# Kernel optimization log

Hardware: AMD Instinct MI355X
Metric: run time of the kernel (lower is better)

## Reference

```python
import jax, jax.numpy as jnp
import numpy as np
from jax import lax

TEMP = 0.1  # softmax_temp default in forward


def _conv(x, w, b):
    y = lax.conv_general_dilated(x, w, (1, 1), 'VALID',
                                 dimension_numbers=('NCHW', 'OIHW', 'NCHW'))
    return y + b[None, :, None, None]


def _avg_pool2(x):
    # AvgPool2d(2,2), floor mode (VALID window)
    s = lax.reduce_window(x, 0.0, lax.add, (1, 1, 2, 2), (1, 1, 2, 2), 'VALID')
    return s / 4.0


def _cnn(x, c1w, c1b, c2w, c2b, c3w, c3b, dw, db):
    x = _avg_pool2(jax.nn.relu(_conv(x, c1w, c1b)))   # (N,8,13,13)
    x = _avg_pool2(jax.nn.relu(_conv(x, c2w, c2b)))   # (N,16,5,5)
    x = _avg_pool2(jax.nn.relu(_conv(x, c3w, c3b)))   # (N,32,1,1)
    x = x.reshape(x.shape[0], -1)                      # (N,32)
    logits = x @ dw.T + db                             # (N,10)
    return jax.nn.softmax(logits, axis=1)


def _digit_to_rule(p):
    # p: (N,10) -> (N,6)
    return jnp.stack([p[:, 8], p[:, 4] + p[:, 6], p[:, 0] + p[:, 2],
                      p[:, 7] + p[:, 9], p[:, 5], p[:, 1] + p[:, 3]], axis=1)


def setup_inputs() -> dict:
    key = jax.random.key(0)
    ks = jax.random.split(key, 10)
    B, T, D, C, H, W = 256, 8, 4, 1, 28, 28
    sc = 0.1
    return {
        'sequences': jax.random.normal(ks[0], (B, T, D, C, H, W), jnp.float32),
        'conv1_w': jax.random.normal(ks[1], (8, 1, 3, 3), jnp.float32) * sc,
        'conv1_b': jax.random.normal(ks[2], (8,), jnp.float32) * sc,
        'conv2_w': jax.random.normal(ks[3], (16, 8, 3, 3), jnp.float32) * sc,
        'conv2_b': jax.random.normal(ks[4], (16,), jnp.float32) * sc,
        'conv3_w': jax.random.normal(ks[5], (32, 16, 3, 3), jnp.float32) * sc,
        'conv3_b': jax.random.normal(ks[6], (32,), jnp.float32) * sc,
        'dense_w': jax.random.normal(ks[7], (10, 32), jnp.float32) * sc,
        'dense_b': jax.random.normal(ks[8], (10,), jnp.float32) * sc,
        'trans': jax.nn.softmax(jax.random.normal(ks[9], (6, 9, 10), jnp.float32), axis=-1),
    }


def reference(sequences, conv1_w, conv1_b, conv2_w, conv2_b, conv3_w, conv3_b,
              dense_w, dense_b, trans):
    B, T, D, C, H, W = sequences.shape
    S = trans.shape[2]           # num_states = 10
    N = T * D                    # number of recurrence steps
    # CNN is independent per (t,d,b): batch all images at once.
    imgs = jnp.transpose(sequences, (1, 2, 0, 3, 4, 5)).reshape(N * B, C, H, W)
    digit_probs = _cnn(imgs, conv1_w, conv1_b, conv2_w, conv2_b,
                       conv3_w, conv3_b, dense_w, dense_b)      # (N*B,10)
    guard_probs = _digit_to_rule(digit_probs)                   # (N*B,6)

    # Per-rule transition matrices: softmax with temperature + fixed accepting row.
    M = jax.nn.softmax(trans / TEMP, axis=-1)                   # (R,S-1,S)
    acc = jnp.zeros((S,), M.dtype).at[-1].set(1.0)
    M = jnp.concatenate([M, jnp.broadcast_to(acc, (M.shape[0], 1, S))], axis=1)  # (R,S,S)

    # Effective transition matrices per step and batch element.
    g = guard_probs.reshape(N, B, -1)
    A_all = jnp.einsum('nbr,rij->nbij', g, M)                   # (N,B,S,S)

    state0 = jnp.zeros((B, S), sequences.dtype).at[:, 0].set(1.0)

    def step(state, A):
        return jnp.einsum('bi,bij->bj', state, A), None

    state_final, _ = lax.scan(step, state0, A_all)
    all_cnn_preds = digit_probs.reshape(N, B, -1)
    all_guard_preds = g
    return all_cnn_preds, all_guard_preds, state_final
```

## Files before the change

kernel.cpp:

```cpp
#include <hip/hip_runtime.h>

typedef _Float16 half_t;
typedef _Float16 h2 __attribute__((ext_vector_type(2)));
typedef _Float16 h4 __attribute__((ext_vector_type(4)));

__device__ __forceinline__ float fdot2f(h2 a, h2 b, float c) {
#if __has_builtin(__builtin_amdgcn_fdot2)
    return __builtin_amdgcn_fdot2(a, b, c, false);
#else
    return c + (float)a.x * (float)b.x + (float)a.y * (float)b.y;
#endif
}

__global__ __launch_bounds__(256) void prep_kernel(
    const float* __restrict__ w2g, const float* __restrict__ w3g,
    const float* __restrict__ wdg, float* __restrict__ wsW)
{
    const int tid = threadIdx.x;
    half_t* w2h = (half_t*)(wsW + 320);
    half_t* w3h = w2h + 1152;
    for (int i = tid; i < 320; i += 256) {
        int j = i >> 5, c2 = i & 31;
        wsW[c2 * 10 + j] = wdg[i];
    }
    for (int i = tid; i < 1152; i += 256) {
        int l = i & 3, c = (i >> 2) & 15, g = (i >> 6) & 1, k = i >> 7;
        w2h[i] = (half_t)w2g[(c * 8 + g * 4 + l) * 9 + k];
    }
    for (int i = tid; i < 4608; i += 256) {
        int l = i & 3, c = (i >> 2) & 31, g = (i >> 7) & 3, k = i >> 9;
        w3h[i] = (half_t)w3g[(c * 16 + g * 4 + l) * 9 + k];
    }
}

__global__ __launch_bounds__(256, 6) void cnn_kernel(
    const float* __restrict__ seq,
    const float* __restrict__ w1g, const float* __restrict__ b1g,
    const float* __restrict__ b2g, const float* __restrict__ b3g,
    const float* __restrict__ bdg, const float* __restrict__ wsW,
    float* __restrict__ out)
{
    __shared__ __align__(16) float  s_img2[4][28][28];
    __shared__ __align__(16) half_t s_p1n[4][2][10][11][4];
    __shared__ __align__(16) half_t s_p2n[4][16][16];
    __shared__ __align__(16) half_t s_w[5760];
    __shared__ float s_p3[4][32];

    const int tid   = threadIdx.x;
    const int mbase = blockIdx.x * 4;
    const float* wdt = wsW;

    {
        const float4* wsrc = (const float4*)(wsW + 320);
        float4* wdst = (float4*)s_w;
        for (int i = tid; i < 720; i += 256) wdst[i] = wsrc[i];
    }
    if (tid < 196) {
        #pragma unroll
        for (int img = 0; img < 4; img++) {
            const int m = mbase + img;
            const int b = m & 255, nn = m >> 8;
            const int t = nn >> 2, dd = nn & 3;
            const float4* s4 = (const float4*)(seq + (((size_t)b * 8 + t) * 4 + dd) * 784);
            float4 v = s4[tid];
            int flat = tid * 4;
            int r  = flat / 28;
            int cb = flat - r * 28;
            int e  = cb >> 1;
            *(float2*)&s_img2[img][r][e]      = make_float2(v.x, v.z);
            *(float2*)&s_img2[img][r][14 + e] = make_float2(v.y, v.w);
        }
    }
    __syncthreads();

    for (int idx = tid; idx < 400; idx += 256) {
        const int img = idx / 100;
        const int rem = idx - img * 100;
        const int y   = rem / 10;
        const int x   = rem - y * 10;
        const int r0  = 2 * y;
        float p[4][4];
        #pragma unroll
        for (int i = 0; i < 4; i++) {
            const float* rp = &s_img2[img][r0 + i][0];
            p[i][0] = rp[x];
            p[i][1] = rp[14 + x];
            p[i][2] = rp[x + 1];
            p[i][3] = rp[15 + x];
        }
        float res[8];
        #pragma unroll
        for (int c = 0; c < 8; c++) {
            float w[9];
            #pragma unroll
            for (int k = 0; k < 9; k++) w[k] = w1g[c * 9 + k];
            const float bias = b1g[c];
            float acc = 0.f;
            #pragma unroll
            for (int rr = 0; rr < 2; rr++)
                #pragma unroll
                for (int cc = 0; cc < 2; cc++) {
                    float v = bias;
                    #pragma unroll
                    for (int i = 0; i < 3; i++)
                        #pragma unroll
                        for (int j = 0; j < 3; j++)
                            v += p[rr + i][cc + j] * w[i * 3 + j];
                    acc += fmaxf(v, 0.f);
                }
            res[c] = 0.25f * acc;
        }
        const int slot = (x >> 1) + 5 * (x & 1);
        h4 lo = { (half_t)res[0], (half_t)res[1], (half_t)res[2], (half_t)res[3] };
        h4 hi = { (half_t)res[4], (half_t)res[5], (half_t)res[6], (half_t)res[7] };
        *(h4*)&s_p1n[img][0][y][slot][0] = lo;
        *(h4*)&s_p1n[img][1][y][slot][0] = hi;
    }
    __syncthreads();

    const int img2 = tid >> 6;
    const int t6   = tid & 63;

    {
        const int pos = t6 >> 2;
        const int q   = t6 & 3;
        const int y   = pos >> 2, x = pos & 3;
        const int r0  = 2 * y;
        const int slotm[4] = { x, 5 + x, x + 1, 6 + x };
        float v[4][4];
        #pragma unroll
        for (int oc = 0; oc < 4; oc++) {
            const float bias = b2g[q * 4 + oc];
            #pragma unroll
            for (int w2 = 0; w2 < 4; w2++) v[oc][w2] = bias;
        }
        #pragma unroll
        for (int g = 0; g < 2; g++) {
            h2 aL[4][4], aH[4][4];
            #pragma unroll
            for (int i = 0; i < 4; i++)
                #pragma unroll
                for (int dx = 0; dx < 4; dx++) {
                    h4 a = *(const h4*)&s_p1n[img2][g][r0 + i][slotm[dx]][0];
                    aL[i][dx] = __builtin_shufflevector(a, a, 0, 1);
                    aH[i][dx] = __builtin_shufflevector(a, a, 2, 3);
                }
            #pragma unroll
            for (int oc = 0; oc < 4; oc++) {
                h4 wk[9];
                #pragma unroll
                for (int k = 0; k < 9; k++)
                    wk[k] = *(const h4*)&s_w[((k * 2 + g) * 16 + q * 4 + oc) * 4];
                #pragma unroll
                for (int k = 0; k < 9; k++) {
                    const int di = k / 3, dj = k - di * 3;
                    h2 wL = __builtin_shufflevector(wk[k], wk[k], 0, 1);
                    h2 wH = __builtin_shufflevector(wk[k], wk[k], 2, 3);
                    #pragma unroll
                    for (int rr = 0; rr < 2; rr++)
                        #pragma unroll
                        for (int cc = 0; cc < 2; cc++) {
                            float* acc = &v[oc][rr * 2 + cc];
                            *acc = fdot2f(aL[rr + di][cc + dj], wL, *acc);
                            *acc = fdot2f(aH[rr + di][cc + dj], wH, *acc);
                        }
                }
            }
        }
        float res[4];
        #pragma unroll
        for (int oc = 0; oc < 4; oc++)
            res[oc] = 0.25f * (fmaxf(v[oc][0], 0.f) + fmaxf(v[oc][1], 0.f) +
                               fmaxf(v[oc][2], 0.f) + fmaxf(v[oc][3], 0.f));
        h4 o = { (half_t)res[0], (half_t)res[1], (half_t)res[2], (half_t)res[3] };
        *(h4*)&s_p2n[img2][pos][q * 4] = o;
    }
    __syncthreads();

    {
        const int c = t6 >> 1;
        const int u = t6 & 1;
        float acc0 = b3g[c], acc1 = acc0;
        #pragma unroll
        for (int g = 0; g < 4; g++) {
            h2 AL[3][4], AH[3][4];
            #pragma unroll
            for (int i = 0; i < 3; i++)
                #pragma unroll
                for (int jj = 0; jj < 4; jj++) {
                    h4 a = *(const h4*)&s_p2n[img2][(u + i) * 4 + jj][g * 4];
                    AL[i][jj] = __builtin_shufflevector(a, a, 0, 1);
                    AH[i][jj] = __builtin_shufflevector(a, a, 2, 3);
                }
            h4 wk[9];
            #pragma unroll
            for (int k = 0; k < 9; k++)
                wk[k] = *(const h4*)&s_w[1152 + ((k * 4 + g) * 32 + c) * 4];
            #pragma unroll
            for (int k = 0; k < 9; k++) {
                const int i = k / 3, j = k - i * 3;
                h2 wL = __builtin_shufflevector(wk[k], wk[k], 0, 1);
                h2 wH = __builtin_shufflevector(wk[k], wk[k], 2, 3);
                acc0 = fdot2f(AL[i][j], wL, acc0);
                acc0 = fdot2f(AH[i][j], wH, acc0);
                acc1 = fdot2f(AL[i][j + 1], wL, acc1);
                acc1 = fdot2f(AH[i][j + 1], wH, acc1);
            }
        }
        float s = fmaxf(acc0, 0.f) + fmaxf(acc1, 0.f);
        s += __shfl_xor(s, 1, 64);
        if (u == 0) s_p3[img2][c] = 0.25f * s;
    }
    __syncthreads();

    {
        float logit = -1e30f;
        if (t6 < 10) {
            float acc = bdg[t6];
            #pragma unroll
            for (int c2 = 0; c2 < 32; c2++) acc += s_p3[img2][c2] * wdt[c2 * 10 + t6];
            logit = acc;
        }
        float mx = logit;
        #pragma unroll
        for (int s = 1; s < 16; s <<= 1) mx = fmaxf(mx, __shfl_xor(mx, s, 16));
        float e = (t6 < 10) ? __expf(logit - mx) : 0.f;
        float ssum = e;
        #pragma unroll
        for (int s = 1; s < 16; s <<= 1) ssum += __shfl_xor(ssum, s, 16);
        float p = e / ssum;
        const int m = mbase + img2;
        if (t6 < 10) out[(size_t)m * 10 + t6] = p;

        const int sh = (t6 < 6 ? t6 : 0) * 4;
        const int ia = (0x157048 >> sh) & 0xF;
        const int ib = (0x3F926F >> sh) & 0xF;
        float pa = __shfl(p, ia, 16);
        float pb = __shfl(p, ib, 16);
        if (t6 < 6)
            out[81920 + (size_t)m * 6 + t6] = pa + pb;
    }
}

__global__ __launch_bounds__(256) void sfa_kernel(
    const float* __restrict__ trans,
    const float* __restrict__ out_guards,
    float* __restrict__ out)
{
    __shared__ float M[600];
    const int tid  = threadIdx.x;
    const int lane = tid & 63;
    const int wv   = tid >> 6;

    if (tid < 54) {
        int r = tid / 9, i = tid - r * 9;
        const float* row = trans + (size_t)(r * 9 + i) * 10;
        float x[10], mx = -1e30f;
        #pragma unroll
        for (int j = 0; j < 10; j++) { x[j] = 10.f * row[j]; mx = fmaxf(mx, x[j]); }
        float s = 0.f;
        #pragma unroll
        for (int j = 0; j < 10; j++) { x[j] = __expf(x[j] - mx); s += x[j]; }
        float inv = 1.f / s;
        #pragma unroll
        for (int j = 0; j < 10; j++) M[(r * 9 + i) * 10 + j] = x[j] * inv;
    }
    __syncthreads();

    const int bb    = lane / 10;
    const int j     = lane - bb * 10;
    const int base  = bb * 10;
    const bool ok   = (bb < 6);
    int batch = blockIdx.x * 24 + wv * 6 + bb;
    const bool live = ok && (batch < 256);
    if (!live) batch = 0;

    float Mreg[54];
    #pragma unroll
    for (int k = 0; k < 54; k++) Mreg[k] = M[k * 10 + j];

    float stj = (j == 0) ? 1.f : 0.f;
    const float* gbase = out_guards + 81920;

    for (int nn = 0; nn < 32; nn++) {
        const float* gp = gbase + ((size_t)nn * 256 + batch) * 6;
        float2 ga = *(const float2*)(gp);
        float2 gb = *(const float2*)(gp + 2);
        float2 gc = *(const float2*)(gp + 4);
        float g[6] = {ga.x, ga.y, gb.x, gb.y, gc.x, gc.y};

        float st[10];
        #pragma unroll
        for (int i = 0; i < 10; i++) st[i] = __shfl(stj, base + i, 64);

        float gsum = g[0] + g[1] + g[2] + g[3] + g[4] + g[5];
        float ns = (j == 9) ? gsum * st[9] : 0.f;
        #pragma unroll
        for (int r = 0; r < 6; r++) {
            float h = 0.f;
            #pragma unroll
            for (int i = 0; i < 9; i++) h += st[i] * Mreg[r * 9 + i];
            ns += g[r] * h;
        }
        stj = ns;
    }
    if (live) out[131072 + (size_t)batch * 10 + j] = stj;
}

extern "C" void kernel_launch(void* const* d_in, const int* in_sizes, int n_in,
                              void* d_out, int out_size, void* d_ws, size_t ws_size,
                              hipStream_t stream) {
    const float* seq = (const float*)d_in[0];
    const float* w1  = (const float*)d_in[1];
    const float* b1  = (const float*)d_in[2];
    const float* w2  = (const float*)d_in[3];
    const float* b2  = (const float*)d_in[4];
    const float* w3  = (const float*)d_in[5];
    const float* b3  = (const float*)d_in[6];
    const float* wd  = (const float*)d_in[7];
    const float* bd  = (const float*)d_in[8];
    const float* tr  = (const float*)d_in[9];
    float* out = (float*)d_out;
    float* wsW = (float*)d_ws;

    prep_kernel<<<1, 256, 0, stream>>>(w2, w3, wd, wsW);
    cnn_kernel<<<2048, 256, 0, stream>>>(seq, w1, b1, b2, b3, bd, wsW, out);
    sfa_kernel<<<11, 256, 0, stream>>>(tr, out, out);
}
```

Before: 139.1 us.

## Compute conv2 with MFMA 16x16x32 f16 instead of packed fdot2

Rewrites the second convolution as an implicit GEMM on the matrix cores using mfma_f32_16x16x32_f16. The weights are pre-packed into a zero-padded B-fragment layout in global workspace, and each lane loads its B fragments directly instead of staging conv2 weights in shared memory. Input patches are gathered per lane with validity masks, and the 2x2 pooling is done through a cross-lane shuffle. The aim is to replace the many fdot2 instructions with a few MFMAs and to shrink shared memory, but the launch-bounds occupancy hint drops from 6 to 4 and the padded K dimension wastes some MFMA work.

```diff
diff --git a/kernel.cpp b/kernel.cpp
--- a/kernel.cpp
+++ b/kernel.cpp
@@ -3,6 +3,8 @@
 typedef _Float16 half_t;
 typedef _Float16 h2 __attribute__((ext_vector_type(2)));
 typedef _Float16 h4 __attribute__((ext_vector_type(4)));
+typedef _Float16 f16x8 __attribute__((ext_vector_type(8)));
+typedef float f32x4 __attribute__((ext_vector_type(4)));
 
 __device__ __forceinline__ float fdot2f(h2 a, h2 b, float c) {
 #if __has_builtin(__builtin_amdgcn_fdot2)
@@ -17,23 +19,35 @@
     const float* __restrict__ wdg, float* __restrict__ wsW)
 {
     const int tid = threadIdx.x;
-    half_t* w2h = (half_t*)(wsW + 320);
-    half_t* w3h = w2h + 1152;
+    half_t* w3h = (half_t*)(wsW + 320);
+    half_t* w2B = (half_t*)(wsW + 2624);
     for (int i = tid; i < 320; i += 256) {
         int j = i >> 5, c2 = i & 31;
         wsW[c2 * 10 + j] = wdg[i];
     }
-    for (int i = tid; i < 1152; i += 256) {
-        int l = i & 3, c = (i >> 2) & 15, g = (i >> 6) & 1, k = i >> 7;
-        w2h[i] = (half_t)w2g[(c * 8 + g * 4 + l) * 9 + k];
-    }
     for (int i = tid; i < 4608; i += 256) {
         int l = i & 3, c = (i >> 2) & 31, g = (i >> 7) & 3, k = i >> 9;
         w3h[i] = (half_t)w3g[(c * 16 + g * 4 + l) * 9 + k];
     }
-}
-
-__global__ __launch_bounds__(256, 6) void cnn_kernel(
+    for (int i = tid; i < 1536; i += 256) {
+        int c    = i >> 9;
+        int r    = i & 511;
+        int lane = r >> 3;
+        int j    = r & 7;
+        int k    = c * 32 + ((lane >> 4) << 3) + j;
+        half_t val = (half_t)0.f;
+        if (k < 72) {
+            int t = k >> 2, l = k & 3;
+            int g = (t >= 9) ? 1 : 0;
+            int tap = t - 9 * g;
+            int oc  = lane & 15;
+            val = (half_t)w2g[(oc * 8 + g * 4 + l) * 9 + tap];
+        }
+        w2B[i] = val;
+    }
+}
+
+__global__ __launch_bounds__(256, 4) void cnn_kernel(
     const float* __restrict__ seq,
     const float* __restrict__ w1g, const float* __restrict__ b1g,
     const float* __restrict__ b2g, const float* __restrict__ b3g,
@@ -43,17 +57,18 @@
     __shared__ __align__(16) float  s_img2[4][28][28];
     __shared__ __align__(16) half_t s_p1n[4][2][10][11][4];
     __shared__ __align__(16) half_t s_p2n[4][16][16];
-    __shared__ __align__(16) half_t s_w[5760];
+    __shared__ __align__(16) half_t s_w[4608];
     __shared__ float s_p3[4][32];
 
     const int tid   = threadIdx.x;
     const int mbase = blockIdx.x * 4;
-    const float* wdt = wsW;
+    const float*  wdt = wsW;
+    const half_t* w2B = (const half_t*)(wsW + 2624);
 
     {
         const float4* wsrc = (const float4*)(wsW + 320);
         float4* wdst = (float4*)s_w;
-        for (int i = tid; i < 720; i += 256) wdst[i] = wsrc[i];
+        for (int i = tid; i < 576; i += 256) wdst[i] = wsrc[i];
     }
     if (tid < 196) {
         #pragma unroll
@@ -122,58 +137,69 @@
     const int t6   = tid & 63;
 
     {
-        const int pos = t6 >> 2;
-        const int q   = t6 & 3;
-        const int y   = pos >> 2, x = pos & 3;
-        const int r0  = 2 * y;
-        const int slotm[4] = { x, 5 + x, x + 1, 6 + x };
-        float v[4][4];
-        #pragma unroll
-        for (int oc = 0; oc < 4; oc++) {
-            const float bias = b2g[q * 4 + oc];
-            #pragma unroll
-            for (int w2 = 0; w2 < 4; w2++) v[oc][w2] = bias;
-        }
-        #pragma unroll
-        for (int g = 0; g < 2; g++) {
-            h2 aL[4][4], aH[4][4];
-            #pragma unroll
-            for (int i = 0; i < 4; i++)
-                #pragma unroll
-                for (int dx = 0; dx < 4; dx++) {
-                    h4 a = *(const h4*)&s_p1n[img2][g][r0 + i][slotm[dx]][0];
-                    aL[i][dx] = __builtin_shufflevector(a, a, 0, 1);
-                    aH[i][dx] = __builtin_shufflevector(a, a, 2, 3);
+        const int q  = t6 >> 4;
+        const int oc = t6 & 15;
+        int tg[6], ti[6], tj[6];
+        bool tv[6];
+        #pragma unroll
+        for (int c = 0; c < 3; c++)
+            #pragma unroll
+            for (int s = 0; s < 2; s++) {
+                int e = c * 2 + s;
+                int t = c * 8 + q * 2 + s;
+                bool v = (t < 18);
+                int tt = v ? t : 0;
+                int g = (tt >= 9) ? 1 : 0;
+                int tap = tt - 9 * g;
+                tg[e] = g; ti[e] = tap / 3; tj[e] = tap - 3 * (tap / 3); tv[e] = v;
+            }
+        f16x8 B[3];
+        #pragma unroll
+        for (int c = 0; c < 3; c++)
+            B[c] = *(const f16x8*)&w2B[(c * 64 + t6) * 8];
+
+        const float bias = b2g[oc];
+        f32x4 acc[4];
+        #pragma unroll
+        for (int T = 0; T < 4; T++) {
+            acc[T][0] = bias; acc[T][1] = bias; acc[T][2] = bias; acc[T][3] = bias;
+        }
+        const int mm = t6 & 15;
+        #pragma unroll
+        for (int T = 0; T < 4; T++) {
+            const int cy = 2 * T + (mm >> 3);
+            const int cx = mm & 7;
+            #pragma unroll
+            for (int c = 0; c < 3; c++) {
+                h4 a0, a1;
+                a0[0]=a0[1]=a0[2]=a0[3]=(half_t)0.f;
+                a1[0]=a1[1]=a1[2]=a1[3]=(half_t)0.f;
+                const int e0 = c * 2, e1 = c * 2 + 1;
+                if (tv[e0]) {
+                    int col = cx + tj[e0];
+                    int slot = (col >> 1) + 5 * (col & 1);
+                    a0 = *(const h4*)&s_p1n[img2][tg[e0]][cy + ti[e0]][slot][0];
                 }
-            #pragma unroll
-            for (int oc = 0; oc < 4; oc++) {
-                h4 wk[9];
-                #pragma unroll
-                for (int k = 0; k < 9; k++)
-                    wk[k] = *(const h4*)&s_w[((k * 2 + g) * 16 + q * 4 + oc) * 4];
-                #pragma unroll
-                for (int k = 0; k < 9; k++) {
-                    const int di = k / 3, dj = k - di * 3;
-                    h2 wL = __builtin_shufflevector(wk[k], wk[k], 0, 1);
-                    h2 wH = __builtin_shufflevector(wk[k], wk[k], 2, 3);
-                    #pragma unroll
-                    for (int rr = 0; rr < 2; rr++)
-                        #pragma unroll
-                        for (int cc = 0; cc < 2; cc++) {
-                            float* acc = &v[oc][rr * 2 + cc];
-                            *acc = fdot2f(aL[rr + di][cc + dj], wL, *acc);
-                            *acc = fdot2f(aH[rr + di][cc + dj], wH, *acc);
-                        }
+                if (tv[e1]) {
+                    int col = cx + tj[e1];
+                    int slot = (col >> 1) + 5 * (col & 1);
+                    a1 = *(const h4*)&s_p1n[img2][tg[e1]][cy + ti[e1]][slot][0];
                 }
+                f16x8 A = __builtin_shufflevector(a0, a1, 0, 1, 2, 3, 4, 5, 6, 7);
+                acc[T] = __builtin_amdgcn_mfma_f32_16x16x32_f16(A, B[c], acc[T], 0, 0, 0);
             }
         }
-        float res[4];
-        #pragma unroll
-        for (int oc = 0; oc < 4; oc++)
-            res[oc] = 0.25f * (fmaxf(v[oc][0], 0.f) + fmaxf(v[oc][1], 0.f) +
-                               fmaxf(v[oc][2], 0.f) + fmaxf(v[oc][3], 0.f));
-        h4 o = { (half_t)res[0], (half_t)res[1], (half_t)res[2], (half_t)res[3] };
-        *(h4*)&s_p2n[img2][pos][q * 4] = o;
+        #pragma unroll
+        for (int T = 0; T < 4; T++) {
+            float p0 = fmaxf(acc[T][0], 0.f) + fmaxf(acc[T][1], 0.f);
+            float p1 = fmaxf(acc[T][2], 0.f) + fmaxf(acc[T][3], 0.f);
+            p0 += __shfl_xor(p0, 32, 64);
+            p1 += __shfl_xor(p1, 32, 64);
+            if (q < 2) {
+                s_p2n[img2][T * 4 + q * 2    ][oc] = (half_t)(0.25f * p0);
+                s_p2n[img2][T * 4 + q * 2 + 1][oc] = (half_t)(0.25f * p1);
+            }
+        }
     }
     __syncthreads();
 
@@ -195,7 +221,7 @@
             h4 wk[9];
             #pragma unroll
             for (int k = 0; k < 9; k++)
-                wk[k] = *(const h4*)&s_w[1152 + ((k * 4 + g) * 32 + c) * 4];
+                wk[k] = *(const h4*)&s_w[((k * 4 + g) * 32 + c) * 4];
             #pragma unroll
             for (int k = 0; k < 9; k++) {
                 const int i = k / 3, j = k - i * 3;
```

New measurement: 136.1 us. 2.2% less time.
